# Kernel optimization log

Measured on AMD Instinct MI355X. Metric: run time of the kernel, lower is better.

## Reference

```python
import jax, jax.numpy as jnp
import numpy as np

DIM = 1024
HEADS = 16
DIM_HEAD = 64
INNER = HEADS * DIM_HEAD
B, N = 2, 2048


def setup_inputs() -> dict:
    key = jax.random.key(0)
    ks = jax.random.split(key, 5)
    x = jax.random.normal(ks[0], (B, N, DIM), dtype=jnp.float32)
    ln_gamma = jnp.ones((DIM,), dtype=jnp.float32)
    ln_beta = jnp.zeros((DIM,), dtype=jnp.float32)
    # torch Linear: weight [out, in]; store as [in, out] for x @ W
    W_qkv = jax.random.normal(ks[1], (DIM, 3 * INNER), dtype=jnp.float32) * (DIM ** -0.5)
    W_out = jax.random.normal(ks[2], (INNER, DIM), dtype=jnp.float32) * (INNER ** -0.5)
    b_out = jax.random.normal(ks[3], (DIM,), dtype=jnp.float32) * 0.01
    return {"x": x, "ln_gamma": ln_gamma, "ln_beta": ln_beta,
            "W_qkv": W_qkv, "W_out": W_out, "b_out": b_out}


def reference(x, ln_gamma, ln_beta, W_qkv, W_out, b_out):
    eps = 1e-5
    scale = DIM_HEAD ** -0.5
    # LayerNorm over last dim
    mu = jnp.mean(x, axis=-1, keepdims=True)
    var = jnp.mean((x - mu) ** 2, axis=-1, keepdims=True)
    xn = (x - mu) * jax.lax.rsqrt(var + eps) * ln_gamma + ln_beta
    # QKV projection (no bias), split
    qkv = xn @ W_qkv                               # [B, N, 3*inner]
    q, k, v = jnp.split(qkv, 3, axis=-1)           # each [B, N, inner]
    def heads(t):
        return t.reshape(B, N, HEADS, DIM_HEAD).transpose(0, 2, 1, 3)  # [B, H, N, d]
    q, k, v = heads(q), heads(k), heads(v)
    dots = jnp.einsum("bhnd,bhmd->bhnm", q, k) * scale
    a = jax.nn.softmax(dots, axis=-1)
    out = jnp.einsum("bhnm,bhmd->bhnd", a, v)      # [B, H, N, d]
    out = out.transpose(0, 2, 1, 3).reshape(B, N, INNER)
    return out @ W_out + b_out                     # dropout p=0 -> identity
```

## Files before the change

kernel.cpp:

```cpp
#include <hip/hip_runtime.h>

typedef unsigned short U16;
typedef __bf16 bf16x8 __attribute__((ext_vector_type(8)));
typedef float f32x4 __attribute__((ext_vector_type(4)));
typedef float f32x16 __attribute__((ext_vector_type(16)));

__device__ inline float b2f(U16 u) {
    union { unsigned int i; float f; } v;
    v.i = ((unsigned int)u) << 16;
    return v.f;
}
__device__ inline U16 f2b(float f) {
    union { float f; unsigned int u; } v;
    v.f = f;
    unsigned int r = (v.u + 0x7fffu + ((v.u >> 16) & 1u)) >> 16;
    return (U16)r;
}

__device__ inline unsigned cvt_pk(float lo, float hi) {
    unsigned d;
    asm("v_cvt_pk_bf16_f32 %0, %1, %2" : "=v"(d) : "v"(lo), "v"(hi));
    return d;
}
__device__ inline void plswap(unsigned &a, unsigned &b) {
    asm("v_permlane32_swap_b32 %0, %1" : "+v"(a), "+v"(b));
}

__device__ inline void gld16(const void* g, void* l) {
    __builtin_amdgcn_global_load_lds(
        (const __attribute__((address_space(1))) void*)g,
        (__attribute__((address_space(3))) void*)l, 16, 0, 0);
}

__global__ void transpose_f2b(const float* __restrict__ in, U16* __restrict__ out,
                              int R, int C) {
    __shared__ float tile[32][33];
    int c0 = blockIdx.x * 32, r0 = blockIdx.y * 32;
    int tx = threadIdx.x, ty = threadIdx.y;
#pragma unroll
    for (int i = 0; i < 32; i += 8)
        tile[ty + i][tx] = in[(size_t)(r0 + ty + i) * C + c0 + tx];
    __syncthreads();
#pragma unroll
    for (int i = 0; i < 32; i += 8)
        out[(size_t)(c0 + ty + i) * R + r0 + tx] = f2b(tile[tx][ty + i]);
}

__global__ __launch_bounds__(256) void ln_kernel(const float* __restrict__ x,
                                                 const float* __restrict__ gamma,
                                                 const float* __restrict__ beta,
                                                 U16* __restrict__ xn) {
    int row = blockIdx.x;
    int t = threadIdx.x;
    float4 raw = ((const float4*)(x + (size_t)row * 1024))[t];
    float v[4] = { raw.x, raw.y, raw.z, raw.w };
    float s = v[0] + v[1] + v[2] + v[3];
    float s2 = v[0] * v[0] + v[1] * v[1] + v[2] * v[2] + v[3] * v[3];
#pragma unroll
    for (int off = 32; off >= 1; off >>= 1) {
        s  += __shfl_xor(s,  off);
        s2 += __shfl_xor(s2, off);
    }
    __shared__ float red[8];
    if ((t & 63) == 0) { red[(t >> 6) * 2] = s; red[(t >> 6) * 2 + 1] = s2; }
    __syncthreads();
    float S  = red[0] + red[2] + red[4] + red[6];
    float S2 = red[1] + red[3] + red[5] + red[7];
    float mu = S * (1.0f / 1024.0f);
    float var = S2 * (1.0f / 1024.0f) - mu * mu;
    float rstd = rsqrtf(var + 1e-5f);
    float4 g4 = ((const float4*)gamma)[t];
    float4 b4 = ((const float4*)beta)[t];
    ushort4 o;
    o.x = f2b((v[0] - mu) * rstd * g4.x + b4.x);
    o.y = f2b((v[1] - mu) * rstd * g4.y + b4.y);
    o.z = f2b((v[2] - mu) * rstd * g4.z + b4.z);
    o.w = f2b((v[3] - mu) * rstd * g4.w + b4.w);
    ((ushort4*)(xn + (size_t)row * 1024))[t] = o;
}

template <typename OutT>
__global__ __launch_bounds__(256) void gemm_bt(const U16* __restrict__ A,
                                               const U16* __restrict__ Bt,
                                               const float* __restrict__ bias,
                                               OutT* __restrict__ C,
                                               U16* __restrict__ vT,
                                               int M, int N, int K) {
    __shared__ __align__(16) U16 As[128 * 32];
    __shared__ __align__(16) U16 Bs[128 * 32];
    const int m0 = blockIdx.y * 128, n0 = blockIdx.x * 128;
    const int t = threadIdx.x;
    const int wave = t >> 6, lane = t & 63, l15 = lane & 15, quad = lane >> 4;
    const int wm = (wave >> 1) * 64, wn = (wave & 1) * 64;

    f32x4 acc[4][4];
#pragma unroll
    for (int i = 0; i < 4; i++)
#pragma unroll
        for (int j = 0; j < 4; j++)
            acc[i][j] = (f32x4){0.f, 0.f, 0.f, 0.f};

    const int c0i = t, c1i = 256 + t;
    const int r0 = c0i >> 2, kq0 = c0i & 3;
    const int r1 = c1i >> 2, kq1 = c1i & 3;

    for (int k0 = 0; k0 < K; k0 += 32) {
        gld16(&A[(size_t)(m0 + r0) * K + k0 + kq0 * 8], &As[c0i * 8]);
        gld16(&Bt[(size_t)(n0 + r0) * K + k0 + kq0 * 8], &Bs[c0i * 8]);
        gld16(&A[(size_t)(m0 + r1) * K + k0 + kq1 * 8], &As[c1i * 8]);
        gld16(&Bt[(size_t)(n0 + r1) * K + k0 + kq1 * 8], &Bs[c1i * 8]);
        __syncthreads();
        bf16x8 af[4], bfr[4];
#pragma unroll
        for (int i = 0; i < 4; i++)
            af[i] = *(const bf16x8*)&As[(wm + i * 16 + l15) * 32 + quad * 8];
#pragma unroll
        for (int j = 0; j < 4; j++)
            bfr[j] = *(const bf16x8*)&Bs[(wn + j * 16 + l15) * 32 + quad * 8];
#pragma unroll
        for (int i = 0; i < 4; i++)
#pragma unroll
            for (int j = 0; j < 4; j++)
                acc[i][j] = __builtin_amdgcn_mfma_f32_16x16x32_bf16(
                    af[i], bfr[j], acc[i][j], 0, 0, 0);
        __syncthreads();
    }
    if (vT && n0 >= 2048) {
#pragma unroll
        for (int i = 0; i < 4; i++) {
#pragma unroll
            for (int j = 0; j < 4; j++) {
                int col = n0 + wn + j * 16 + l15 - 2048;
                int hh = col >> 6, dd = col & 63;
                int row0 = m0 + wm + i * 16 + quad * 4;
                int bb = row0 >> 11, nn = row0 & 2047;
                ushort4 st;
                st.x = f2b(acc[i][j][0]); st.y = f2b(acc[i][j][1]);
                st.z = f2b(acc[i][j][2]); st.w = f2b(acc[i][j][3]);
                *(ushort4*)&vT[((((size_t)bb * 16) + hh) * 64 + dd) * 2048 + nn] = st;
            }
        }
        return;
    }
#pragma unroll
    for (int i = 0; i < 4; i++) {
#pragma unroll
        for (int j = 0; j < 4; j++) {
            int col = n0 + wn + j * 16 + l15;
            float bv = bias ? bias[col] : 0.0f;
#pragma unroll
            for (int r = 0; r < 4; r++) {
                int row = m0 + wm + i * 16 + quad * 4 + r;
                float val = acc[i][j][r] + bv;
                if constexpr (sizeof(OutT) == 4)
                    C[(size_t)row * N + col] = val;
                else
                    C[(size_t)row * N + col] = f2b(val);
            }
        }
    }
}

__global__ __launch_bounds__(256) void attn_kernel(const U16* __restrict__ qkv,
                                                   const U16* __restrict__ vT,
                                                   U16* __restrict__ attn_out) {
    const int p = blockIdx.x;
    const int xcd = p & 7;
    const int slot = p >> 3;
    const int bh = ((slot & 3) << 3) | xcd;
    const int qt = slot >> 2;
    const int b = bh >> 4, h = bh & 15;
    const int t = threadIdx.x;
    const int wave = t >> 6, lane = t & 63;
    const int l31 = lane & 31, hi = lane >> 5;
    const float sc2 = 0.125f * 1.44269504089f;

    __shared__ __align__(16) U16 Kt[2][64 * 64];
    __shared__ __align__(16) U16 Vt[2][64 * 64];

    const size_t base = (size_t)(b * 2048) * 3072;
    const U16* vTbh = vT + ((size_t)(b * 16 + h) * 64) * 2048;

    bf16x8 qf[4];
    {
        int qrow = qt * 128 + wave * 32 + l31;
        const U16* qp = qkv + base + (size_t)qrow * 3072 + h * 64 + hi * 8;
#pragma unroll
        for (int s = 0; s < 4; s++)
            qf[s] = *(const bf16x8*)&qp[s * 16];
    }

    float l_acc = 0.0f;
    f32x16 oacc[2];
#pragma unroll
    for (int db = 0; db < 2; db++)
#pragma unroll
        for (int r = 0; r < 16; r++)
            oacc[db][r] = 0.0f;

    const int c0 = t, c1 = 256 + t;
    const int row0 = c0 >> 3, oct0 = (c0 & 7) ^ (row0 & 7);
    const int row1 = c1 >> 3, oct1 = (c1 & 7) ^ (row1 & 7);

    gld16(&qkv[base + (size_t)row0 * 3072 + 1024 + h * 64 + oct0 * 8], &Kt[0][c0 * 8]);
    gld16(&qkv[base + (size_t)row1 * 3072 + 1024 + h * 64 + oct1 * 8], &Kt[0][c1 * 8]);
    gld16(&vTbh[(size_t)row0 * 2048 + oct0 * 8], &Vt[0][c0 * 8]);
    gld16(&vTbh[(size_t)row1 * 2048 + oct1 * 8], &Vt[0][c1 * 8]);
    __syncthreads();

    for (int kt = 0; kt < 32; kt++) {
        {
            int nt = (kt + 1) & 31, nb = (kt + 1) & 1;
            gld16(&qkv[base + (size_t)(nt * 64 + row0) * 3072 + 1024 + h * 64 + oct0 * 8], &Kt[nb][c0 * 8]);
            gld16(&qkv[base + (size_t)(nt * 64 + row1) * 3072 + 1024 + h * 64 + oct1 * 8], &Kt[nb][c1 * 8]);
            gld16(&vTbh[(size_t)row0 * 2048 + nt * 64 + oct0 * 8], &Vt[nb][c0 * 8]);
            gld16(&vTbh[(size_t)row1 * 2048 + nt * 64 + oct1 * 8], &Vt[nb][c1 * 8]);
        }
        const U16* KtC = &Kt[kt & 1][0];
        const U16* VtC = &Vt[kt & 1][0];

#pragma unroll
        for (int kb = 0; kb < 2; kb++) {
            bf16x8 kf[4];
#pragma unroll
            for (int s = 0; s < 4; s++)
                kf[s] = *(const bf16x8*)&KtC[(kb * 32 + l31) * 64 +
                                             (((s * 2 + hi) ^ (l31 & 7)) * 8)];
            bf16x8 vfr[2][2];
#pragma unroll
            for (int db = 0; db < 2; db++)
#pragma unroll
                for (int s = 0; s < 2; s++)
                    vfr[db][s] = *(const bf16x8*)&VtC[(db * 32 + l31) * 64 +
                                                      (((kb * 4 + s * 2 + hi) ^ (l31 & 7)) * 8)];

            f32x16 st = {0.f, 0.f, 0.f, 0.f, 0.f, 0.f, 0.f, 0.f,
                         0.f, 0.f, 0.f, 0.f, 0.f, 0.f, 0.f, 0.f};
            __builtin_amdgcn_s_setprio(1);
#pragma unroll
            for (int s = 0; s < 4; s++)
                st = __builtin_amdgcn_mfma_f32_32x32x16_bf16(kf[s], qf[s], st, 0, 0, 0);
            __builtin_amdgcn_s_setprio(0);

            float pe[16];
#pragma unroll
            for (int r = 0; r < 16; r++) {
                pe[r] = __builtin_amdgcn_exp2f(st[r] * sc2);
                l_acc += pe[r];
            }

#pragma unroll
            for (int s = 0; s < 2; s++) {
                unsigned p01 = cvt_pk(pe[s * 8 + 0], pe[s * 8 + 1]);
                unsigned p23 = cvt_pk(pe[s * 8 + 2], pe[s * 8 + 3]);
                unsigned p45 = cvt_pk(pe[s * 8 + 4], pe[s * 8 + 5]);
                unsigned p67 = cvt_pk(pe[s * 8 + 6], pe[s * 8 + 7]);
                plswap(p01, p45);
                plswap(p23, p67);
                union { unsigned u[4]; bf16x8 v; } pw;
                pw.u[0] = p01; pw.u[1] = p23; pw.u[2] = p45; pw.u[3] = p67;
                __builtin_amdgcn_s_setprio(1);
#pragma unroll
                for (int db = 0; db < 2; db++)
                    oacc[db] = __builtin_amdgcn_mfma_f32_32x32x16_bf16(
                        vfr[db][s], pw.v, oacc[db], 0, 0, 0);
                __builtin_amdgcn_s_setprio(0);
            }
        }
        __syncthreads();
    }

    float lt = l_acc + __shfl_xor(l_acc, 32);
    float inv = 1.0f / lt;
    int qrow = b * 2048 + qt * 128 + wave * 32 + l31;
#pragma unroll
    for (int db = 0; db < 2; db++) {
#pragma unroll
        for (int g = 0; g < 4; g++) {
            ushort4 stv;
            stv.x = f2b(oacc[db][g * 4 + 0] * inv);
            stv.y = f2b(oacc[db][g * 4 + 1] * inv);
            stv.z = f2b(oacc[db][g * 4 + 2] * inv);
            stv.w = f2b(oacc[db][g * 4 + 3] * inv);
            int col = h * 64 + db * 32 + g * 8 + hi * 4;
            *(ushort4*)&attn_out[(size_t)qrow * 1024 + col] = stv;
        }
    }
}

extern "C" void kernel_launch(void* const* d_in, const int* in_sizes, int n_in,
                              void* d_out, int out_size, void* d_ws, size_t ws_size,
                              hipStream_t stream) {
    (void)in_sizes; (void)n_in; (void)out_size; (void)ws_size;
    const float* x    = (const float*)d_in[0];
    const float* g    = (const float*)d_in[1];
    const float* be   = (const float*)d_in[2];
    const float* Wqkv = (const float*)d_in[3];
    const float* Wout = (const float*)d_in[4];
    const float* bout = (const float*)d_in[5];
    float* out = (float*)d_out;
    char* ws = (char*)d_ws;

    U16* xn   = (U16*)(ws);
    U16* qkv  = (U16*)(ws + (size_t)(8u  << 20));
    U16* WqT  = (U16*)(ws + (size_t)(32u << 20));
    U16* WoT  = (U16*)(ws + (size_t)(38u << 20));
    U16* vT   = (U16*)(ws + (size_t)(40u << 20));
    U16* aout = xn;

    transpose_f2b<<<dim3(3072 / 32, 1024 / 32), dim3(32, 8), 0, stream>>>(Wqkv, WqT, 1024, 3072);
    transpose_f2b<<<dim3(1024 / 32, 1024 / 32), dim3(32, 8), 0, stream>>>(Wout, WoT, 1024, 1024);
    ln_kernel<<<4096, 256, 0, stream>>>(x, g, be, xn);
    gemm_bt<U16><<<dim3(3072 / 128, 4096 / 128), 256, 0, stream>>>(xn, WqT, nullptr, qkv, vT, 4096, 3072, 1024);
    attn_kernel<<<dim3(512), 256, 0, stream>>>(qkv, vT, aout);
    gemm_bt<float><<<dim3(1024 / 128, 4096 / 128), 256, 0, stream>>>(aout, WoT, bout, out, nullptr, 4096, 1024, 1024);
}
```

Before: 207.8 us.

## Split attention key range in two halves and merge partial outputs

The attention kernel now launches twice as many blocks, each covering half of the key/value sequence. Each block writes unnormalised fp32 partial outputs and per-head row sums, and a new merge kernel adds the two halves, normalises them and converts to bf16. The aim is more parallelism and better CU occupancy for attention. The cost is an extra kernel launch and extra fp32 global-memory traffic for the partial buffers. The merge only sums the partials without rescaling, so it relies on both halves using the same softmax offset.

Measured after the change: 216.3 us. 1.04x slower.

```diff
diff --git a/kernel.cpp b/kernel.cpp
--- a/kernel.cpp
+++ b/kernel.cpp
@@ -163,12 +163,16 @@
 
 __global__ __launch_bounds__(256) void attn_kernel(const U16* __restrict__ qkv,
                                                    const U16* __restrict__ vT,
-                                                   U16* __restrict__ attn_out) {
+                                                   float* __restrict__ po0,
+                                                   float* __restrict__ po1,
+                                                   float* __restrict__ pl) {
     const int p = blockIdx.x;
     const int xcd = p & 7;
     const int slot = p >> 3;
     const int bh = ((slot & 3) << 3) | xcd;
-    const int qt = slot >> 2;
+    const int r2 = slot >> 2;
+    const int qt = r2 & 15;
+    const int half = r2 >> 4;
     const int b = bh >> 4, h = bh & 15;
     const int t = threadIdx.x;
     const int wave = t >> 6, lane = t & 63;
@@ -180,6 +184,7 @@
 
     const size_t base = (size_t)(b * 2048) * 3072;
     const U16* vTbh = vT + ((size_t)(b * 16 + h) * 64) * 2048;
+    const int kbase = half * 16;
 
     bf16x8 qf[4];
     {
@@ -202,22 +207,25 @@
     const int row0 = c0 >> 3, oct0 = (c0 & 7) ^ (row0 & 7);
     const int row1 = c1 >> 3, oct1 = (c1 & 7) ^ (row1 & 7);
 
-    gld16(&qkv[base + (size_t)row0 * 3072 + 1024 + h * 64 + oct0 * 8], &Kt[0][c0 * 8]);
-    gld16(&qkv[base + (size_t)row1 * 3072 + 1024 + h * 64 + oct1 * 8], &Kt[0][c1 * 8]);
-    gld16(&vTbh[(size_t)row0 * 2048 + oct0 * 8], &Vt[0][c0 * 8]);
-    gld16(&vTbh[(size_t)row1 * 2048 + oct1 * 8], &Vt[0][c1 * 8]);
+    {
+        int nt = kbase;
+        gld16(&qkv[base + (size_t)(nt * 64 + row0) * 3072 + 1024 + h * 64 + oct0 * 8], &Kt[0][c0 * 8]);
+        gld16(&qkv[base + (size_t)(nt * 64 + row1) * 3072 + 1024 + h * 64 + oct1 * 8], &Kt[0][c1 * 8]);
+        gld16(&vTbh[(size_t)row0 * 2048 + nt * 64 + oct0 * 8], &Vt[0][c0 * 8]);
+        gld16(&vTbh[(size_t)row1 * 2048 + nt * 64 + oct1 * 8], &Vt[0][c1 * 8]);
+    }
     __syncthreads();
 
-    for (int kt = 0; kt < 32; kt++) {
+    for (int i = 0; i < 16; i++) {
         {
-            int nt = (kt + 1) & 31, nb = (kt + 1) & 1;
+            int nt = kbase + ((i + 1) & 15), nb = (i + 1) & 1;
             gld16(&qkv[base + (size_t)(nt * 64 + row0) * 3072 + 1024 + h * 64 + oct0 * 8], &Kt[nb][c0 * 8]);
             gld16(&qkv[base + (size_t)(nt * 64 + row1) * 3072 + 1024 + h * 64 + oct1 * 8], &Kt[nb][c1 * 8]);
             gld16(&vTbh[(size_t)row0 * 2048 + nt * 64 + oct0 * 8], &Vt[nb][c0 * 8]);
             gld16(&vTbh[(size_t)row1 * 2048 + nt * 64 + oct1 * 8], &Vt[nb][c1 * 8]);
         }
-        const U16* KtC = &Kt[kt & 1][0];
-        const U16* VtC = &Vt[kt & 1][0];
+        const U16* KtC = &Kt[i & 1][0];
+        const U16* VtC = &Vt[i & 1][0];
 
 #pragma unroll
         for (int kb = 0; kb < 2; kb++) {
@@ -270,22 +278,42 @@
         __syncthreads();
     }
 
-    float lt = l_acc + __shfl_xor(l_acc, 32);
-    float inv = 1.0f / lt;
+    float lh = l_acc + __shfl_xor(l_acc, 32);
+    float* po_h = half ? po1 : po0;
     int qrow = b * 2048 + qt * 128 + wave * 32 + l31;
 #pragma unroll
     for (int db = 0; db < 2; db++) {
 #pragma unroll
         for (int g = 0; g < 4; g++) {
-            ushort4 stv;
-            stv.x = f2b(oacc[db][g * 4 + 0] * inv);
-            stv.y = f2b(oacc[db][g * 4 + 1] * inv);
-            stv.z = f2b(oacc[db][g * 4 + 2] * inv);
-            stv.w = f2b(oacc[db][g * 4 + 3] * inv);
+            float4 stv;
+            stv.x = oacc[db][g * 4 + 0];
+            stv.y = oacc[db][g * 4 + 1];
+            stv.z = oacc[db][g * 4 + 2];
+            stv.w = oacc[db][g * 4 + 3];
             int col = h * 64 + db * 32 + g * 8 + hi * 4;
-            *(ushort4*)&attn_out[(size_t)qrow * 1024 + col] = stv;
-        }
-    }
+            *(float4*)&po_h[(size_t)qrow * 1024 + col] = stv;
+        }
+    }
+    if (hi == 0)
+        pl[((size_t)half * 4096 + qrow) * 16 + h] = lh;
+}
+
+__global__ __launch_bounds__(256) void merge_kernel(const float* __restrict__ po0,
+                                                    const float* __restrict__ po1,
+                                                    const float* __restrict__ pl,
+                                                    U16* __restrict__ aout) {
+    int row = blockIdx.x;
+    int t = threadIdx.x;
+    int h = t >> 4;
+    float inv = 1.0f / (pl[(size_t)row * 16 + h] + pl[((size_t)4096 + row) * 16 + h]);
+    float4 a = ((const float4*)(po0 + (size_t)row * 1024))[t];
+    float4 c = ((const float4*)(po1 + (size_t)row * 1024))[t];
+    ushort4 o;
+    o.x = f2b((a.x + c.x) * inv);
+    o.y = f2b((a.y + c.y) * inv);
+    o.z = f2b((a.z + c.z) * inv);
+    o.w = f2b((a.w + c.w) * inv);
+    ((ushort4*)(aout + (size_t)row * 1024))[t] = o;
 }
 
 extern "C" void kernel_launch(void* const* d_in, const int* in_sizes, int n_in,
@@ -306,12 +334,16 @@
     U16* WqT  = (U16*)(ws + (size_t)(32u << 20));
     U16* WoT  = (U16*)(ws + (size_t)(38u << 20));
     U16* vT   = (U16*)(ws + (size_t)(40u << 20));
+    float* po1 = (float*)(ws + (size_t)(48u << 20));
+    float* pl  = (float*)(ws + (size_t)(64u << 20));
     U16* aout = xn;
+    float* po0 = out;
 
     transpose_f2b<<<dim3(3072 / 32, 1024 / 32), dim3(32, 8), 0, stream>>>(Wqkv, WqT, 1024, 3072);
     transpose_f2b<<<dim3(1024 / 32, 1024 / 32), dim3(32, 8), 0, stream>>>(Wout, WoT, 1024, 1024);
     ln_kernel<<<4096, 256, 0, stream>>>(x, g, be, xn);
     gemm_bt<U16><<<dim3(3072 / 128, 4096 / 128), 256, 0, stream>>>(xn, WqT, nullptr, qkv, vT, 4096, 3072, 1024);
-    attn_kernel<<<dim3(512), 256, 0, stream>>>(qkv, vT, aout);
+    attn_kernel<<<dim3(1024), 256, 0, stream>>>(qkv, vT, po0, po1, pl);
+    merge_kernel<<<dim3(4096), 256, 0, stream>>>(po0, po1, pl, aout);
     gemm_bt<float><<<dim3(1024 / 128, 4096 / 128), 256, 0, stream>>>(aout, WoT, bout, out, nullptr, 4096, 1024, 1024);
 }
```
